# Optimization experiments

Hardware: AMD Instinct MI355X
Metric: run time of the kernel (lower is better)

The kernel has to match this reference:

```python
import jax, jax.numpy as jnp
import numpy as np

MASK_LOGIT_CONST = 1000000000.0
LN_EPS = 1e-12


def setup_inputs() -> dict:
    key = jax.random.key(0)
    k_in, k_w = jax.random.split(key)
    B, S, H = 8, 2048, 1024
    inputs = jax.random.normal(k_in, (B, S, H), dtype=jnp.float32)
    masks = jnp.ones((B, S, S), dtype=jnp.float32)
    w_match = jax.random.normal(k_w, (2 * H, H), dtype=jnp.float32) * (1.0 / np.sqrt(2 * H))
    b_match = jnp.zeros((H,), dtype=jnp.float32)
    ln_gamma = jnp.ones((H,), dtype=jnp.float32)
    ln_beta = jnp.zeros((H,), dtype=jnp.float32)
    return {"inputs": inputs, "masks": masks, "w_match": w_match,
            "b_match": b_match, "ln_gamma": ln_gamma, "ln_beta": ln_beta}


def reference(inputs, masks, w_match, b_match, ln_gamma, ln_beta):
    H = inputs.shape[-1]
    scale = 1.0 / jnp.sqrt(jnp.asarray(H, dtype=inputs.dtype))
    # self-attention scores [B,S,S] (dropout disabled -> query=key=inputs)
    scores = jnp.einsum('bsh,bth->bst', inputs, inputs) * scale
    # logits_mask: scores*mask + (-C)*(1-mask)
    scores = scores * masks - MASK_LOGIT_CONST * (1.0 - masks)
    probs = jax.nn.softmax(scores, axis=-1)
    context = jnp.einsum('bst,bth->bsh', probs, inputs)
    cat = jnp.concatenate([inputs, context], axis=-1)  # [B,S,2H]
    matching = jnp.einsum('bsk,kh->bsh', cat, w_match) + b_match
    # layernorm over last dim
    mu = jnp.mean(matching, axis=-1, keepdims=True)
    var = jnp.mean((matching - mu) ** 2, axis=-1, keepdims=True)
    normed = (matching - mu) * jax.lax.rsqrt(var + LN_EPS)
    return normed * ln_gamma + ln_beta
```

## Files before the change

### kernel.cpp

```cpp
#include <hip/hip_runtime.h>
#include <hip/hip_bf16.h>
#include <hip/hip_fp8.h>


typedef unsigned short ushort_t;
typedef __attribute__((ext_vector_type(8))) short short8;
typedef __attribute__((ext_vector_type(4))) float float4v;

__device__ inline float b2f(unsigned int u) {
    union { unsigned int i; float f; } v; v.i = u << 16; return v.f;
}
__device__ inline ushort_t f2b(float f) {
    __hip_bfloat16 h = __float2bfloat16(f);
    return __builtin_bit_cast(ushort_t, h);
}
__device__ inline unsigned char f2e4(float f) {
    return __hip_fp8_e4m3(f).__x;
}

__device__ inline void gload_lds16(const void* g, void* lds) {
    __builtin_amdgcn_global_load_lds(
        (const __attribute__((address_space(1))) unsigned int*)g,
        (__attribute__((address_space(3))) unsigned int*)lds, 16, 0, 0);
}

#define BM 128
#define BN 128
#define BK 64

template<int EPI>
__global__ __launch_bounds__(256, 2)
void gemm_bt(const ushort_t* __restrict__ A, const ushort_t* __restrict__ A2, int kSplit,
             const ushort_t* __restrict__ B,
             int M, int N, int K, int lda, int ldb, int ldc,
             long aBS, long bBS, long cBS,
             const float* __restrict__ rowsum,
             const float* __restrict__ bias,
             ushort_t* __restrict__ outb)
{
    __shared__ __align__(16) ushort_t As[BM * BK];
    __shared__ __align__(16) ushort_t Bs[BN * BK];

    const int tid = threadIdx.x;
    const int z = blockIdx.z;
    A  += (size_t)z * aBS;
    A2 += (size_t)z * aBS;
    B  += (size_t)z * bBS;
    if (EPI == 2) rowsum += (size_t)z * M;
    outb += (size_t)z * cBS;

    const int bm = blockIdx.x * BM;
    const int bn = blockIdx.y * BN;
    const int wave = tid >> 6, lane = tid & 63;
    const int wm = (wave >> 1) * 64, wn = (wave & 1) * 64;
    const int q = lane >> 4, l15 = lane & 15;
    const int lrow = lane >> 3;
    const int cswz = (lane & 7) ^ lrow;

    float4v acc[4][4];
#pragma unroll
    for (int i = 0; i < 4; i++)
#pragma unroll
        for (int j = 0; j < 4; j++) acc[i][j] = (float4v){0.f, 0.f, 0.f, 0.f};

    for (int k0 = 0; k0 < K; k0 += BK) {
        const ushort_t* aSrc = A;
        int ka = k0;
        if (k0 >= kSplit) { aSrc = A2; ka = k0 - kSplit; }
#pragma unroll
        for (int j = 0; j < 4; j++) {
            const int p = wave * 4 + j;
            const int ro = p * 8 + lrow;
            gload_lds16(aSrc + (size_t)(bm + ro) * lda + ka + cswz * 8, &As[p * 512]);
            gload_lds16(B    + (size_t)(bn + ro) * ldb + k0 + cswz * 8, &Bs[p * 512]);
        }
        __syncthreads();
#pragma unroll
        for (int kk = 0; kk < BK; kk += 32) {
            short8 af[4], bfv[4];
            const int kc = (kk >> 3) + q;
#pragma unroll
            for (int mi = 0; mi < 4; mi++) {
                const int lr = wm + mi * 16 + l15;
                af[mi] = *(const short8*)(&As[lr * 64 + ((kc ^ (lr & 7)) << 3)]);
            }
#pragma unroll
            for (int ni = 0; ni < 4; ni++) {
                const int lr = wn + ni * 16 + l15;
                bfv[ni] = *(const short8*)(&Bs[lr * 64 + ((kc ^ (lr & 7)) << 3)]);
            }
#pragma unroll
            for (int mi = 0; mi < 4; mi++)
#pragma unroll
                for (int ni = 0; ni < 4; ni++)
                    acc[mi][ni] = __builtin_amdgcn_mfma_f32_16x16x32_bf16(
                        af[mi], bfv[ni], acc[mi][ni], 0, 0, 0);
        }
        __syncthreads();
    }

#pragma unroll
    for (int mi = 0; mi < 4; mi++) {
#pragma unroll
        for (int r = 0; r < 4; r++) {
            const int row = bm + wm + mi * 16 + q * 4 + r;
            const size_t ro = (size_t)row * ldc;
            float rsinv = 1.f;
            if (EPI == 2) rsinv = 1.0f / rowsum[row];
#pragma unroll
            for (int ni = 0; ni < 4; ni++) {
                const int col = bn + wn + ni * 16 + l15;
                float v = acc[mi][ni][r];
                if (EPI == 2) outb[ro + col] = f2b(v * rsinv);
                else          outb[ro + col] = f2b(v + bias[col]);
            }
        }
    }
}

__global__ __launch_bounds__(256, 2)
void gemm1_fp8(const unsigned char* __restrict__ X8,
               const float* __restrict__ mask,
               float* __restrict__ rowsum,
               ushort_t* __restrict__ E)
{
    __shared__ __align__(16) unsigned char As[128 * 128];
    __shared__ __align__(16) unsigned char Bs[128 * 128];

    const int tid = threadIdx.x;
    const int z = blockIdx.z;
    const unsigned char* Xz = X8 + (size_t)z * 2048 * 1024;
    const float* mz = mask + (size_t)z * 2048 * 2048;
    float* rsz = rowsum + (size_t)z * 2048;
    ushort_t* Ez = E + (size_t)z * 2048 * 2048;

    const int bm = blockIdx.x * 128;
    const int bn = blockIdx.y * 128;
    const int wave = tid >> 6, lane = tid & 63;
    const int wm = (wave >> 1) * 64, wn = (wave & 1) * 64;
    const int q = lane >> 4, l15 = lane & 15;
    const int rx = l15 & 7;
    const int lrow = lane >> 3;
    const int cswz = (lane & 7) ^ lrow;

    float4v acc[4][4];
#pragma unroll
    for (int i = 0; i < 4; i++)
#pragma unroll
        for (int j = 0; j < 4; j++) acc[i][j] = (float4v){0.f, 0.f, 0.f, 0.f};

    for (int k0 = 0; k0 < 1024; k0 += 128) {
#pragma unroll
        for (int j = 0; j < 4; j++) {
            const int p = wave * 4 + j;
            const int ro = p * 8 + lrow;
            gload_lds16(Xz + (size_t)(bm + ro) * 1024 + k0 + cswz * 16, &As[p * 1024]);
            gload_lds16(Xz + (size_t)(bn + ro) * 1024 + k0 + cswz * 16, &Bs[p * 1024]);
        }
        __syncthreads();
#pragma unroll
        for (int kk = 0; kk < 128; kk += 32) {
            const int g = (kk >> 3) + q;
            const int co = (((g >> 1) ^ rx) << 4) + ((g & 1) << 3);
            long af[4], bfv[4];
#pragma unroll
            for (int mi = 0; mi < 4; mi++)
                af[mi] = *(const long*)(&As[(wm + mi * 16 + l15) * 128 + co]);
#pragma unroll
            for (int ni = 0; ni < 4; ni++)
                bfv[ni] = *(const long*)(&Bs[(wn + ni * 16 + l15) * 128 + co]);
#pragma unroll
            for (int mi = 0; mi < 4; mi++)
#pragma unroll
                for (int ni = 0; ni < 4; ni++)
                    acc[mi][ni] = __builtin_amdgcn_mfma_f32_16x16x32_fp8_fp8(
                        af[mi], bfv[ni], acc[mi][ni], 0, 0, 0);
        }
        __syncthreads();
    }

    const float scale = 0.03125f;
#pragma unroll
    for (int mi = 0; mi < 4; mi++) {
#pragma unroll
        for (int r = 0; r < 4; r++) {
            const int row = bm + wm + mi * 16 + q * 4 + r;
            const size_t ro = (size_t)row * 2048;
            float s = 0.f;
#pragma unroll
            for (int ni = 0; ni < 4; ni++) {
                const int col = bn + wn + ni * 16 + l15;
                const float m = mz[ro + col];
                float v = __expf(acc[mi][ni][r] * scale * m - 1e9f * (1.0f - m));
                s += v;
                Ez[ro + col] = f2b(v);
            }
            s += __shfl_xor(s, 8);
            s += __shfl_xor(s, 4);
            s += __shfl_xor(s, 2);
            s += __shfl_xor(s, 1);
            if (l15 == 0) atomicAdd(&rsz[row], s);
        }
    }
}

__global__ __launch_bounds__(256)
void conv_trans(const float* __restrict__ in, ushort_t* __restrict__ outT,
                ushort_t* __restrict__ outS, unsigned char* __restrict__ outQ,
                int R, int C)
{
    __shared__ float tile[64][65];
    const int tx = threadIdx.x & 15, ty = threadIdx.x >> 4;
    const size_t zoff = (size_t)blockIdx.z * R * C;
    const int r0 = blockIdx.y * 64, c0 = blockIdx.x * 64;
#pragma unroll
    for (int j = 0; j < 4; j++) {
        const int r = ty + j * 16;
        const float4 v = *(const float4*)(in + zoff + (size_t)(r0 + r) * C + c0 + tx * 4);
        tile[r][tx * 4 + 0] = v.x;
        tile[r][tx * 4 + 1] = v.y;
        tile[r][tx * 4 + 2] = v.z;
        tile[r][tx * 4 + 3] = v.w;
        if (outS) {
            ushort4 o;
            o.x = f2b(v.x); o.y = f2b(v.y); o.z = f2b(v.z); o.w = f2b(v.w);
            *(ushort4*)(outS + zoff + (size_t)(r0 + r) * C + c0 + tx * 4) = o;
            uchar4 p;
            p.x = f2e4(v.x); p.y = f2e4(v.y); p.z = f2e4(v.z); p.w = f2e4(v.w);
            *(uchar4*)(outQ + zoff + (size_t)(r0 + r) * C + c0 + tx * 4) = p;
        }
    }
    __syncthreads();
    ushort_t* tp = outT + zoff;
#pragma unroll
    for (int j = 0; j < 4; j++) {
        const int cc = ty + j * 16;
        ushort4 o;
        o.x = f2b(tile[tx * 4 + 0][cc]);
        o.y = f2b(tile[tx * 4 + 1][cc]);
        o.z = f2b(tile[tx * 4 + 2][cc]);
        o.w = f2b(tile[tx * 4 + 3][cc]);
        *(ushort4*)(tp + (size_t)(c0 + cc) * R + r0 + tx * 4) = o;
    }
}

__global__ __launch_bounds__(256)
void ln_k(const ushort_t* __restrict__ Mt, const float* __restrict__ gamma,
          const float* __restrict__ beta, float* __restrict__ out)
{
    const size_t row = blockIdx.x;
    const int tid = threadIdx.x;
    const ushort4 u = *(const ushort4*)(Mt + row * 1024 + tid * 4);
    float x0 = b2f(u.x), x1 = b2f(u.y), x2 = b2f(u.z), x3 = b2f(u.w);
    float s  = x0 + x1 + x2 + x3;
    float s2 = x0 * x0 + x1 * x1 + x2 * x2 + x3 * x3;
#pragma unroll
    for (int off = 32; off > 0; off >>= 1) {
        s  += __shfl_down(s, off);
        s2 += __shfl_down(s2, off);
    }
    __shared__ float red[8];
    const int wave = tid >> 6, lane = tid & 63;
    if (lane == 0) { red[wave] = s; red[4 + wave] = s2; }
    __syncthreads();
    s  = red[0] + red[1] + red[2] + red[3];
    s2 = red[4] + red[5] + red[6] + red[7];
    const float mu  = s * (1.0f / 1024.0f);
    const float var = s2 * (1.0f / 1024.0f) - mu * mu;
    const float rinv = rsqrtf(var + 1e-12f);
    const float4 g = *(const float4*)(gamma + tid * 4);
    const float4 b = *(const float4*)(beta + tid * 4);
    float4 o;
    o.x = (x0 - mu) * rinv * g.x + b.x;
    o.y = (x1 - mu) * rinv * g.y + b.y;
    o.z = (x2 - mu) * rinv * g.z + b.z;
    o.w = (x3 - mu) * rinv * g.w + b.w;
    *(float4*)(out + row * 1024 + tid * 4) = o;
}

extern "C" void kernel_launch(void* const* d_in, const int* in_sizes, int n_in,
                              void* d_out, int out_size, void* d_ws, size_t ws_size,
                              hipStream_t stream)
{
    const float* X     = (const float*)d_in[0];
    const float* masks = (const float*)d_in[1];
    const float* Wm    = (const float*)d_in[2];
    const float* bias  = (const float*)d_in[3];
    const float* gamma = (const float*)d_in[4];
    const float* beta  = (const float*)d_in[5];
    float* out = (float*)d_out;
    char* ws = (char*)d_ws;

    const int B = 8, S = 2048, H = 1024;

    ushort_t* Xb  = (ushort_t*)(ws);
    ushort_t* XT  = (ushort_t*)(ws + 33554432);
    ushort_t* WT  = (ushort_t*)(ws + 67108864);
    ushort_t* E   = (ushort_t*)(ws + 71303168);
    float*    rs  = (float*)   (ws + 138412032);
    ushort_t* CTX = (ushort_t*)(ws + 138477568);
    unsigned char* X8 = (unsigned char*)CTX;
    ushort_t* matching = E;

    conv_trans<<<dim3(16, 32, 8), 256, 0, stream>>>(X, XT, Xb, X8, S, H);
    conv_trans<<<dim3(16, 32, 1), 256, 0, stream>>>(Wm, WT, nullptr, nullptr, 2 * H, H);
    hipMemsetAsync(rs, 0, (size_t)B * S * sizeof(float), stream);

    gemm1_fp8<<<dim3(16, 16, 8), 256, 0, stream>>>(X8, masks, rs, E);

    gemm_bt<2><<<dim3(16, 8, 8), 256, 0, stream>>>(
        E, E, 1 << 30, XT,
        S, H, S, S, S, H,
        (long)S * S, (long)H * S, (long)S * H,
        rs, nullptr, CTX);

    gemm_bt<3><<<dim3(128, 8, 1), 256, 0, stream>>>(
        Xb, CTX, H, WT,
        B * S, H, 2 * H, H, 2 * H, H,
        0, 0, 0,
        nullptr, bias, matching);

    ln_k<<<B * S, 256, 0, stream>>>(matching, gamma, beta, out);
}
```

Before: 504.8 us.

## Rewrite bf16 GEMM with 256x256 tiles, 8 waves and 4-stage LDS pipeline

The bf16 GEMM kernel moves from 128x128 tiles with 4 waves and a single LDS buffer to 256x256 tiles with 8 waves, BK=32, and a four-deep ring of LDS buffers. Async global-to-LDS loads are issued three stages ahead, gated by explicit vmcnt waits and barriers, and MFMA priority is raised with setprio. The goal is to hide global load latency and get more MFMA work per byte loaded. In exchange it uses 128KB of LDS and more accumulator registers per wave, which lowers occupancy and leaves fewer blocks in the grid to fill the CUs.

```diff
diff --git a/kernel.cpp b/kernel.cpp
--- a/kernel.cpp
+++ b/kernel.cpp
@@ -24,12 +24,8 @@
         (__attribute__((address_space(3))) unsigned int*)lds, 16, 0, 0);
 }
 
-#define BM 128
-#define BN 128
-#define BK 64
-
 template<int EPI>
-__global__ __launch_bounds__(256, 2)
+__global__ __launch_bounds__(512, 2)
 void gemm_bt(const ushort_t* __restrict__ A, const ushort_t* __restrict__ A2, int kSplit,
              const ushort_t* __restrict__ B,
              int M, int N, int K, int lda, int ldb, int ldc,
@@ -38,8 +34,7 @@
              const float* __restrict__ bias,
              ushort_t* __restrict__ outb)
 {
-    __shared__ __align__(16) ushort_t As[BM * BK];
-    __shared__ __align__(16) ushort_t Bs[BN * BK];
+    __shared__ __align__(16) ushort_t smem[4 * 16384];
 
     const int tid = threadIdx.x;
     const int z = blockIdx.z;
@@ -49,58 +44,72 @@
     if (EPI == 2) rowsum += (size_t)z * M;
     outb += (size_t)z * cBS;
 
-    const int bm = blockIdx.x * BM;
-    const int bn = blockIdx.y * BN;
-    const int wave = tid >> 6, lane = tid & 63;
-    const int wm = (wave >> 1) * 64, wn = (wave & 1) * 64;
+    const int bm = blockIdx.x * 256;
+    const int bn = blockIdx.y * 256;
+    const int w = tid >> 6, lane = tid & 63;
+    const int wm = (w >> 2) * 128, wn = (w & 3) * 64;
     const int q = lane >> 4, l15 = lane & 15;
-    const int lrow = lane >> 3;
-    const int cswz = (lane & 7) ^ lrow;
-
-    float4v acc[4][4];
-#pragma unroll
-    for (int i = 0; i < 4; i++)
+    const int srow = lane >> 2;
+    const int schunk = ((lane & 3) ^ ((lane >> 3) & 3)) * 8;
+
+    float4v acc[8][4];
+#pragma unroll
+    for (int i = 0; i < 8; i++)
 #pragma unroll
         for (int j = 0; j < 4; j++) acc[i][j] = (float4v){0.f, 0.f, 0.f, 0.f};
 
-    for (int k0 = 0; k0 < K; k0 += BK) {
-        const ushort_t* aSrc = A;
-        int ka = k0;
-        if (k0 >= kSplit) { aSrc = A2; ka = k0 - kSplit; }
-#pragma unroll
-        for (int j = 0; j < 4; j++) {
-            const int p = wave * 4 + j;
-            const int ro = p * 8 + lrow;
-            gload_lds16(aSrc + (size_t)(bm + ro) * lda + ka + cswz * 8, &As[p * 512]);
-            gload_lds16(B    + (size_t)(bn + ro) * ldb + k0 + cswz * 8, &Bs[p * 512]);
-        }
-        __syncthreads();
-#pragma unroll
-        for (int kk = 0; kk < BK; kk += 32) {
-            short8 af[4], bfv[4];
-            const int kc = (kk >> 3) + q;
-#pragma unroll
-            for (int mi = 0; mi < 4; mi++) {
-                const int lr = wm + mi * 16 + l15;
-                af[mi] = *(const short8*)(&As[lr * 64 + ((kc ^ (lr & 7)) << 3)]);
-            }
-#pragma unroll
-            for (int ni = 0; ni < 4; ni++) {
-                const int lr = wn + ni * 16 + l15;
-                bfv[ni] = *(const short8*)(&Bs[lr * 64 + ((kc ^ (lr & 7)) << 3)]);
-            }
-#pragma unroll
-            for (int mi = 0; mi < 4; mi++)
-#pragma unroll
-                for (int ni = 0; ni < 4; ni++)
-                    acc[mi][ni] = __builtin_amdgcn_mfma_f32_16x16x32_bf16(
-                        af[mi], bfv[ni], acc[mi][ni], 0, 0, 0);
-        }
-        __syncthreads();
-    }
-
-#pragma unroll
-    for (int mi = 0; mi < 4; mi++) {
+    const int NT = K >> 5;
+
+#define STAGE(T) do {                                                               \
+        const int k0_ = (T) * 32;                                                   \
+        const ushort_t* aS_ = A; int ka_ = k0_;                                     \
+        if (k0_ >= kSplit) { aS_ = A2; ka_ = k0_ - kSplit; }                        \
+        ushort_t* buf_ = &smem[((T) & 3) * 16384];                                  \
+        gload_lds16(aS_ + (size_t)(bm + w * 16       + srow) * lda + ka_ + schunk,  \
+                    buf_ + w * 512);                                                \
+        gload_lds16(aS_ + (size_t)(bm + (w + 8) * 16 + srow) * lda + ka_ + schunk,  \
+                    buf_ + (w + 8) * 512);                                          \
+        gload_lds16(B   + (size_t)(bn + w * 16       + srow) * ldb + k0_ + schunk,  \
+                    buf_ + 8192 + w * 512);                                         \
+        gload_lds16(B   + (size_t)(bn + (w + 8) * 16 + srow) * ldb + k0_ + schunk,  \
+                    buf_ + 8192 + (w + 8) * 512);                                   \
+    } while (0)
+
+    STAGE(0); STAGE(1); STAGE(2);
+
+    for (int T = 0; T < NT; ++T) {
+        if (T + 2 < NT)      asm volatile("s_waitcnt vmcnt(8)\n\ts_barrier" ::: "memory");
+        else if (T + 1 < NT) asm volatile("s_waitcnt vmcnt(4)\n\ts_barrier" ::: "memory");
+        else                 asm volatile("s_waitcnt vmcnt(0)\n\ts_barrier" ::: "memory");
+
+        if (T + 3 < NT) STAGE(T + 3);
+
+        const ushort_t* bufA = &smem[(T & 3) * 16384];
+        const ushort_t* bufB = bufA + 8192;
+        short8 af[8], bf[4];
+#pragma unroll
+        for (int mi = 0; mi < 8; mi++) {
+            const int r = wm + mi * 16 + l15;
+            af[mi] = *(const short8*)(&bufA[r * 32 + ((q ^ ((r >> 1) & 3)) << 3)]);
+        }
+#pragma unroll
+        for (int ni = 0; ni < 4; ni++) {
+            const int r = wn + ni * 16 + l15;
+            bf[ni] = *(const short8*)(&bufB[r * 32 + ((q ^ ((r >> 1) & 3)) << 3)]);
+        }
+        __builtin_amdgcn_s_setprio(1);
+#pragma unroll
+        for (int mi = 0; mi < 8; mi++)
+#pragma unroll
+            for (int ni = 0; ni < 4; ni++)
+                acc[mi][ni] = __builtin_amdgcn_mfma_f32_16x16x32_bf16(
+                    af[mi], bf[ni], acc[mi][ni], 0, 0, 0);
+        __builtin_amdgcn_s_setprio(0);
+    }
+#undef STAGE
+
+#pragma unroll
+    for (int mi = 0; mi < 8; mi++) {
 #pragma unroll
         for (int r = 0; r < 4; r++) {
             const int row = bm + wm + mi * 16 + q * 4 + r;
@@ -308,13 +317,13 @@
 
     gemm1_fp8<<<dim3(16, 16, 8), 256, 0, stream>>>(X8, masks, rs, E);
 
-    gemm_bt<2><<<dim3(16, 8, 8), 256, 0, stream>>>(
+    gemm_bt<2><<<dim3(8, 4, 8), 512, 0, stream>>>(
         E, E, 1 << 30, XT,
         S, H, S, S, S, H,
         (long)S * S, (long)H * S, (long)S * H,
         rs, nullptr, CTX);
 
-    gemm_bt<3><<<dim3(128, 8, 1), 256, 0, stream>>>(
+    gemm_bt<3><<<dim3(64, 4, 1), 512, 0, stream>>>(
         Xb, CTX, H, WT,
         B * S, H, 2 * H, H, 2 * H, H,
         0, 0, 0,
```

Result: faster. 480.8 us (-4.7%).
